# Performance work log

Hardware: AMD Instinct MI355X
Metric: run time of the kernel (lower is better)

The kernel has to match this reference:

```python
import jax, jax.numpy as jnp
import numpy as np

B, S, D, H = 1, 2048, 2048, 16
HD = D // H  # head_dim = 128
EPS = 1e-6


def setup_inputs() -> dict:
    key = jax.random.key(0)
    ks = jax.random.split(key, 12)
    sc = 0.02
    x = jax.random.normal(ks[0], (B, S, D), jnp.float32)
    wq = jax.random.normal(ks[1], (D, D), jnp.float32) * sc
    bq = jnp.zeros((D,), jnp.float32)
    wk = jax.random.normal(ks[2], (D, D), jnp.float32) * sc
    bk = jnp.zeros((D,), jnp.float32)
    wv = jax.random.normal(ks[3], (D, D), jnp.float32) * sc
    bv = jnp.zeros((D,), jnp.float32)
    wo = jax.random.normal(ks[4], (D, D), jnp.float32) * sc
    bo = jnp.zeros((D,), jnp.float32)
    gq = jnp.ones((D,), jnp.float32)  # RMSNorm weight for q
    gk = jnp.ones((D,), jnp.float32)  # RMSNorm weight for k
    # Rotary frequency table: complex freqs = cos + i*sin, shape [S, 1, HD//2]
    pos = jnp.arange(S, dtype=jnp.float32)
    inv = 1.0 / (10000.0 ** (jnp.arange(0, HD, 2, dtype=jnp.float32) / HD))  # [HD//2]
    theta = pos[:, None] * inv[None, :]  # [S, HD//2]
    freqs_cos = jnp.cos(theta)[:, None, :]  # [S, 1, HD//2]
    freqs_sin = jnp.sin(theta)[:, None, :]
    return {"x": x, "wq": wq, "bq": bq, "wk": wk, "bk": bk, "wv": wv, "bv": bv,
            "wo": wo, "bo": bo, "gq": gq, "gk": gk,
            "freqs_cos": freqs_cos, "freqs_sin": freqs_sin}


def _rmsnorm(x, g):
    # RMSNorm over full model dim (applied BEFORE head split, as in source)
    return x * jax.lax.rsqrt(jnp.mean(x * x, axis=-1, keepdims=True) + EPS) * g


def _rope(x, cos, sin):
    # x: [B,S,D] -> (B,S,H,HD//2,2) complex pairs; complex mult by (cos + i sin)
    b, s, d = x.shape
    xr = x.reshape(b, s, H, HD // 2, 2)
    a, bb = xr[..., 0], xr[..., 1]
    # cos/sin [S,1,HD//2] broadcast against [B,S,H,HD//2]
    ra = a * cos - bb * sin
    rb = a * sin + bb * cos
    return jnp.stack([ra, rb], axis=-1).reshape(b, s, d)


def reference(x, wq, bq, wk, bk, wv, bv, wo, bo, gq, gk, freqs_cos, freqs_sin):
    b, s, d = x.shape
    q = _rope(_rmsnorm(x @ wq.T + bq, gq), freqs_cos, freqs_sin)
    k = _rope(_rmsnorm(x @ wk.T + bk, gk), freqs_cos, freqs_sin)
    v = x @ wv.T + bv
    qh = q.reshape(b, s, H, HD).transpose(0, 2, 1, 3)  # [B,H,S,HD]
    kh = k.reshape(b, s, H, HD).transpose(0, 2, 1, 3)
    vh = v.reshape(b, s, H, HD).transpose(0, 2, 1, 3)
    scores = jnp.einsum('bhqd,bhkd->bhqk', qh, kh) / np.sqrt(HD).astype(np.float32)
    attn = jax.nn.softmax(scores, axis=-1)
    out = jnp.einsum('bhqk,bhkd->bhqd', attn, vh)
    out = out.transpose(0, 2, 1, 3).reshape(b, s, d)
    return out @ wo.T + bo
```

## Files before the change

kernel.cpp:

```cpp
#include <hip/hip_runtime.h>
#include <math.h>

typedef unsigned short u16;
typedef unsigned int u32;
typedef __bf16 bf16x8 __attribute__((ext_vector_type(8)));
typedef float f32x4 __attribute__((ext_vector_type(4)));
typedef float f32x16 __attribute__((ext_vector_type(16)));

__device__ __forceinline__ u16 f2bf(float f) {
  unsigned u = __float_as_uint(f);
  u += 0x7fff + ((u >> 16) & 1);
  return (u16)(u >> 16);
}

__device__ __forceinline__ u32 cvtpk(float lo, float hi) {
  u32 r;
  asm("v_cvt_pk_bf16_f32 %0, %1, %2" : "=v"(r) : "v"(lo), "v"(hi));
  return r;
}

__device__ __forceinline__ void pswap(u32& x, u32& y) {
  asm volatile("v_permlane32_swap_b32 %0, %1" : "+v"(x), "+v"(y));
}

__device__ __forceinline__ void gload_lds16(const void* g, void* l) {
  __builtin_amdgcn_global_load_lds(
      (const __attribute__((address_space(1))) unsigned int*)g,
      (__attribute__((address_space(3))) unsigned int*)l, 16, 0, 0);
}

__global__ __launch_bounds__(256) void k_cvt5(const float* __restrict__ s0,
                                              const float* __restrict__ s1,
                                              const float* __restrict__ s2,
                                              const float* __restrict__ s3,
                                              const float* __restrict__ s4,
                                              u16* __restrict__ dx,
                                              u16* __restrict__ dqkv,
                                              u16* __restrict__ dwo) {
  const int y = blockIdx.y;
  const float* s = (y == 0) ? s0 : (y == 1) ? s1 : (y == 2) ? s2
                   : (y == 3) ? s3 : s4;
  u16* d = (y == 0) ? dx : (y == 4) ? dwo : dqkv + (size_t)(y - 1) * 4194304;
  int i = (blockIdx.x * 256 + threadIdx.x) * 4;
  float4 v = *(const float4*)(s + i);
  ushort4 o;
  o.x = f2bf(v.x); o.y = f2bf(v.y); o.z = f2bf(v.z); o.w = f2bf(v.w);
  *(ushort4*)(d + i) = o;
}

__global__ __launch_bounds__(512, 4) void k_gemm_big(const u16* __restrict__ A,
                                                     const u16* __restrict__ B,
                                                     float* __restrict__ C,
                                                     int M, int N, int K) {
  __shared__ __align__(16) char lds[2][40960];
  const int tid = threadIdx.x;
  const int wid = tid >> 6, lane = tid & 63;
  const int lr = lane & 15, lg = lane >> 4;
  const int wm = (wid >> 2) * 64, wn = (wid & 3) * 48;
  const int nbx = N / 192, nby = M >> 7;
  const int colsPerXcd = nbx >> 3;
  const int xcd = blockIdx.x & 7, idx = blockIdx.x >> 3;
  const int bx = xcd * colsPerXcd + idx / nby;
  const int by = idx % nby;
  const int bm = by * 128, bn = bx * 192;
  const int srow = tid >> 3;
  const int schunk = (tid & 7) ^ (srow & 7);
  const size_t rsK = (size_t)K * 2;
  const char* gA = (const char*)A + (size_t)(bm + srow) * rsK + schunk * 16;
  const char* gB = (const char*)B + (size_t)(bn + srow) * rsK + schunk * 16;
  char* dA = (char*)lds + wid * 1024;
  char* dB = (char*)lds + 16384 + wid * 1024;

#define STAGE(cur, k0)                                                         \
  {                                                                            \
    _Pragma("unroll") for (int i = 0; i < 2; ++i)                              \
        gload_lds16(gA + (size_t)(i * 64) * rsK + (size_t)(k0) * 2,            \
                    dA + (cur) * 40960 + i * 8192);                            \
    _Pragma("unroll") for (int i = 0; i < 3; ++i)                              \
        gload_lds16(gB + (size_t)(i * 64) * rsK + (size_t)(k0) * 2,            \
                    dB + (cur) * 40960 + i * 8192);                            \
  }

  f32x4 acc[4][3] = {};
  STAGE(0, 0);
  STAGE(1, 64);
  asm volatile("s_waitcnt vmcnt(5)" ::: "memory");
  __builtin_amdgcn_s_barrier();
  const int NT = K >> 6;
  int cur = 0;
  const int rsw = (lr & 7);
  for (int t = 0; t < NT; ++t) {
    const char* La = (const char*)lds + cur * 40960;
    const char* Lb = La + 16384;
    bf16x8 af[4][2], bfr[3][2];
#pragma unroll
    for (int mi = 0; mi < 4; ++mi)
#pragma unroll
      for (int kk = 0; kk < 2; ++kk)
        af[mi][kk] = *(const bf16x8*)(La + (wm + mi * 16 + lr) * 128 +
                                      (((kk * 4 + lg) ^ rsw) * 16));
#pragma unroll
    for (int ni = 0; ni < 3; ++ni)
#pragma unroll
      for (int kk = 0; kk < 2; ++kk)
        bfr[ni][kk] = *(const bf16x8*)(Lb + (wn + ni * 16 + lr) * 128 +
                                       (((kk * 4 + lg) ^ rsw) * 16));
    asm volatile("s_waitcnt lgkmcnt(0)" ::: "memory");
    __builtin_amdgcn_s_barrier();
    if (t + 2 < NT) STAGE(cur, (t + 2) << 6);
    __builtin_amdgcn_s_setprio(1);
#pragma unroll
    for (int kk = 0; kk < 2; ++kk)
#pragma unroll
      for (int mi = 0; mi < 4; ++mi)
#pragma unroll
        for (int ni = 0; ni < 3; ++ni)
          acc[mi][ni] = __builtin_amdgcn_mfma_f32_16x16x32_bf16(
              af[mi][kk], bfr[ni][kk], acc[mi][ni], 0, 0, 0);
    __builtin_amdgcn_s_setprio(0);
    if (t + 2 < NT)
      asm volatile("s_waitcnt vmcnt(5)" ::: "memory");
    else
      asm volatile("s_waitcnt vmcnt(0)" ::: "memory");
    __builtin_amdgcn_s_barrier();
    cur ^= 1;
  }
#undef STAGE
#pragma unroll
  for (int mi = 0; mi < 4; ++mi)
#pragma unroll
    for (int ni = 0; ni < 3; ++ni)
#pragma unroll
      for (int j = 0; j < 4; ++j)
        C[(size_t)(bm + wm + mi * 16 + lg * 4 + j) * N + bn + wn + ni * 16 + lr] =
            acc[mi][ni][j];
}

__global__ __launch_bounds__(256, 2) void k_gemm_pipe(const u16* __restrict__ A,
                                                      const u16* __restrict__ B,
                                                      const float* __restrict__ bias,
                                                      float* __restrict__ C,
                                                      int M, int N, int K) {
  __shared__ __align__(16) char lds[2][24576];
  const int tid = threadIdx.x;
  const int wid = tid >> 6, lane = tid & 63;
  const int lr = lane & 15, lg = lane >> 4;
  const int wm = (wid >> 1) * 64, wn = (wid & 1) * 32;
  const int nbx = N >> 6, nby = M >> 7;
  const int colsPerXcd = nbx >> 3;
  const int xcd = blockIdx.x & 7, idx = blockIdx.x >> 3;
  const int bx = xcd * colsPerXcd + idx / nby;
  const int by = idx % nby;
  const int bm = by * 128, bn = bx * 64;
  const int srow = tid >> 3;
  const int schunk = (tid & 7) ^ (srow & 7);
  const size_t rsK = (size_t)K * 2;
  const char* gA = (const char*)A + (size_t)(bm + srow) * rsK + schunk * 16;
  const char* gB = (const char*)B + (size_t)(bn + srow) * rsK + schunk * 16;
  char* dA = (char*)lds + wid * 1024;
  char* dB = (char*)lds + 16384 + wid * 1024;

#define STAGE(cur, k0)                                                         \
  {                                                                            \
    _Pragma("unroll") for (int i = 0; i < 4; ++i)                              \
        gload_lds16(gA + (size_t)(i * 32) * rsK + (size_t)(k0) * 2,            \
                    dA + (cur) * 24576 + i * 4096);                            \
    _Pragma("unroll") for (int i = 0; i < 2; ++i)                              \
        gload_lds16(gB + (size_t)(i * 32) * rsK + (size_t)(k0) * 2,            \
                    dB + (cur) * 24576 + i * 4096);                            \
  }

  f32x4 acc[4][2] = {};
  STAGE(0, 0);
  STAGE(1, 64);
  asm volatile("s_waitcnt vmcnt(6)" ::: "memory");
  __builtin_amdgcn_s_barrier();
  const int NT = K >> 6;
  int cur = 0;
  const int rsw = (lr & 7);
  for (int t = 0; t < NT; ++t) {
    const char* La = (const char*)lds + cur * 24576;
    const char* Lb = La + 16384;
    bf16x8 af[4][2], bfr[2][2];
#pragma unroll
    for (int mi = 0; mi < 4; ++mi)
#pragma unroll
      for (int kk = 0; kk < 2; ++kk)
        af[mi][kk] = *(const bf16x8*)(La + (wm + mi * 16 + lr) * 128 +
                                      (((kk * 4 + lg) ^ rsw) * 16));
#pragma unroll
    for (int ni = 0; ni < 2; ++ni)
#pragma unroll
      for (int kk = 0; kk < 2; ++kk)
        bfr[ni][kk] = *(const bf16x8*)(Lb + (wn + ni * 16 + lr) * 128 +
                                       (((kk * 4 + lg) ^ rsw) * 16));
    asm volatile("s_waitcnt lgkmcnt(0)" ::: "memory");
    __builtin_amdgcn_s_barrier();
    if (t + 2 < NT) STAGE(cur, (t + 2) << 6);
    __builtin_amdgcn_s_setprio(1);
#pragma unroll
    for (int kk = 0; kk < 2; ++kk)
#pragma unroll
      for (int mi = 0; mi < 4; ++mi)
#pragma unroll
        for (int ni = 0; ni < 2; ++ni)
          acc[mi][ni] = __builtin_amdgcn_mfma_f32_16x16x32_bf16(
              af[mi][kk], bfr[ni][kk], acc[mi][ni], 0, 0, 0);
    __builtin_amdgcn_s_setprio(0);
    if (t + 2 < NT)
      asm volatile("s_waitcnt vmcnt(6)" ::: "memory");
    else
      asm volatile("s_waitcnt vmcnt(0)" ::: "memory");
    __builtin_amdgcn_s_barrier();
    cur ^= 1;
  }
#undef STAGE
#pragma unroll
  for (int mi = 0; mi < 4; ++mi)
#pragma unroll
    for (int ni = 0; ni < 2; ++ni) {
      int col = bn + wn + ni * 16 + lr;
      float bb = bias[col];
#pragma unroll
      for (int j = 0; j < 4; ++j)
        C[(size_t)(bm + wm + mi * 16 + lg * 4 + j) * N + col] =
            acc[mi][ni][j] + bb;
    }
}

__global__ __launch_bounds__(256) void k_rmsnorm_rope(
    const float* __restrict__ qkv, const float* __restrict__ bq,
    const float* __restrict__ bk, const float* __restrict__ gq,
    const float* __restrict__ gk, const float* __restrict__ fcos,
    const float* __restrict__ fsin, u16* __restrict__ qb, u16* __restrict__ kb) {
  const int s = blockIdx.x, which = blockIdx.y;
  const int t = threadIdx.x;
  const float* src = qkv + (size_t)s * 6144 + which * 2048;
  const float* bias = which ? bk : bq;
  const float* g = which ? gk : gq;
  u16* dst = (which ? kb : qb) + (size_t)s * 2048;
  const int c0 = t * 8;
  float4 a0 = *(const float4*)(src + c0);
  float4 a1 = *(const float4*)(src + c0 + 4);
  float4 b0 = *(const float4*)(bias + c0);
  float4 b1 = *(const float4*)(bias + c0 + 4);
  float v[8];
  v[0] = a0.x + b0.x; v[1] = a0.y + b0.y; v[2] = a0.z + b0.z; v[3] = a0.w + b0.w;
  v[4] = a1.x + b1.x; v[5] = a1.y + b1.y; v[6] = a1.z + b1.z; v[7] = a1.w + b1.w;
  float ss = 0.f;
#pragma unroll
  for (int j = 0; j < 8; ++j) ss += v[j] * v[j];
#pragma unroll
  for (int m = 1; m < 64; m <<= 1) ss += __shfl_xor(ss, m);
  __shared__ float red[4];
  if ((t & 63) == 0) red[t >> 6] = ss;
  __syncthreads();
  float r = rsqrtf((red[0] + red[1] + red[2] + red[3]) * (1.0f / 2048.0f) + 1e-6f);
  if (!which) r *= 0.08838834764831843f * 1.4426950408889634f;
  float4 g0 = *(const float4*)(g + c0);
  float4 g1 = *(const float4*)(g + c0 + 4);
  float gg[8] = {g0.x, g0.y, g0.z, g0.w, g1.x, g1.y, g1.z, g1.w};
  const int p0 = (c0 & 127) >> 1;
  u16 o[8];
#pragma unroll
  for (int j = 0; j < 4; ++j) {
    float a = v[2 * j] * r * gg[2 * j];
    float b = v[2 * j + 1] * r * gg[2 * j + 1];
    float co = fcos[s * 64 + p0 + j], si = fsin[s * 64 + p0 + j];
    o[2 * j]     = f2bf(a * co - b * si);
    o[2 * j + 1] = f2bf(a * si + b * co);
  }
  ushort4 q0; q0.x = o[0]; q0.y = o[1]; q0.z = o[2]; q0.w = o[3];
  ushort4 q1; q1.x = o[4]; q1.y = o[5]; q1.z = o[6]; q1.w = o[7];
  *(ushort4*)(dst + c0) = q0;
  *(ushort4*)(dst + c0 + 4) = q1;
}

__global__ __launch_bounds__(256) void k_transpose_v(const float* __restrict__ qkv,
                                                     const float* __restrict__ bv,
                                                     u16* __restrict__ vT) {
  __shared__ float tile[64][65];
  const int s0 = blockIdx.x * 64, d0 = blockIdx.y * 64;
  const int t = threadIdx.x;
  const int tc = (t & 15) * 4, tr = t >> 4;
  float4 bb = *(const float4*)(bv + d0 + tc);
#pragma unroll
  for (int i = 0; i < 4; ++i) {
    int sr = tr + i * 16;
    float4 x = *(const float4*)(qkv + (size_t)(s0 + sr) * 6144 + 4096 + d0 + tc);
    tile[sr][tc + 0] = x.x + bb.x;
    tile[sr][tc + 1] = x.y + bb.y;
    tile[sr][tc + 2] = x.z + bb.z;
    tile[sr][tc + 3] = x.w + bb.w;
  }
  __syncthreads();
#pragma unroll
  for (int i = 0; i < 4; ++i) {
    int dr = tr + i * 16;
    ushort4 o;
    o.x = f2bf(tile[tc + 0][dr]);
    o.y = f2bf(tile[tc + 1][dr]);
    o.z = f2bf(tile[tc + 2][dr]);
    o.w = f2bf(tile[tc + 3][dr]);
    *(ushort4*)(vT + (size_t)(d0 + dr) * 2048 + s0 + tc) = o;
  }
}

__global__ __launch_bounds__(256, 2) void k_attn(const u16* __restrict__ qb,
                                                 const u16* __restrict__ kb,
                                                 const u16* __restrict__ vT,
                                                 float* __restrict__ opart,
                                                 float* __restrict__ ml) {
  __shared__ __align__(16) char Ks[2][16384];
  __shared__ __align__(16) char Vs[2][16384];
  const int bid = blockIdx.x;
  const int xcd = bid & 7, j = bid >> 3;
  const int h = xcd * 2 + (j & 1);
  const int qt = (j >> 1) & 15;
  const int ks = j >> 5;
  const int tid = threadIdx.x;
  const int wid = tid >> 6, lane = tid & 63;
  const int l31 = lane & 31, hi = lane >> 5;
  const int q0w = qt * 128 + wid * 32;
  const char* kbB = (const char*)kb;
  const char* vTB = (const char*)vT;
  const int krow = tid >> 4;
  const int kc = (tid & 15) ^ krow;
  const int vrow = tid >> 3;
  const int vc = (tid & 7) ^ (vrow & 7);

#define STAGE(buf, k0)                                                         \
  {                                                                            \
    _Pragma("unroll") for (int i = 0; i < 4; ++i)                              \
        gload_lds16(kbB + (size_t)((k0) + i * 16 + krow) * 4096 + h * 256 +    \
                        kc * 16,                                               \
                    (char*)Ks + (buf) * 16384 + i * 4096 + wid * 1024);        \
    _Pragma("unroll") for (int i = 0; i < 4; ++i)                              \
        gload_lds16(vTB + (size_t)(h * 128 + i * 32 + vrow) * 4096 +           \
                        (size_t)(k0) * 2 + vc * 16,                            \
                    (char*)Vs + (buf) * 16384 + i * 4096 + wid * 1024);        \
  }

  bf16x8 qf[8];
#pragma unroll
  for (int ds = 0; ds < 8; ++ds)
    qf[ds] = *(const bf16x8*)(qb + (size_t)(q0w + l31) * 2048 + h * 128 +
                              ds * 16 + hi * 8);
  f32x16 o[4] = {};
  float mrun = -3.0e38f, lsum = 0.f;
  const int kbeg = ks * 1024;
  const int ksw = l31 & 15, vsw = l31 & 7;
  STAGE(0, kbeg);
  __syncthreads();
  int cur = 0;
  for (int t = 0; t < 16; ++t) {
    if (t + 1 < 16) STAGE(cur ^ 1, kbeg + (t + 1) * 64);
    const char* Kc = Ks[cur];
    const char* Vc = Vs[cur];
    f32x16 p0 = {}, p1 = {};
    __builtin_amdgcn_s_setprio(1);
#pragma unroll
    for (int ds = 0; ds < 8; ++ds) {
      bf16x8 kf0 = *(const bf16x8*)(Kc + l31 * 256 + (((ds * 2 + hi) ^ ksw) * 16));
      p0 = __builtin_amdgcn_mfma_f32_32x32x16_bf16(kf0, qf[ds], p0, 0, 0, 0);
      bf16x8 kf1 = *(const bf16x8*)(Kc + (32 + l31) * 256 +
                                    (((ds * 2 + hi) ^ ksw) * 16));
      p1 = __builtin_amdgcn_mfma_f32_32x32x16_bf16(kf1, qf[ds], p1, 0, 0, 0);
    }
    __builtin_amdgcn_s_setprio(0);
    {
      float tm[8];
#pragma unroll
      for (int r = 0; r < 8; ++r)
        tm[r] = fmaxf(fmaxf(p0[2 * r], p0[2 * r + 1]),
                      fmaxf(p1[2 * r], p1[2 * r + 1]));
#pragma unroll
      for (int s = 4; s > 0; s >>= 1)
#pragma unroll
        for (int r = 0; r < s; ++r) tm[r] = fmaxf(tm[r], tm[r + s]);
      float pm = fmaxf(tm[0], __shfl_xor(tm[0], 32));
      if (!__all(pm <= mrun + 8.0f)) {
        float nm = fmaxf(mrun, pm);
        float fv = __builtin_amdgcn_exp2f(mrun - nm);
#pragma unroll
        for (int dt = 0; dt < 4; ++dt) o[dt] *= fv;
        lsum *= fv;
        mrun = nm;
      }
    }
    {
#pragma unroll
      for (int r = 0; r < 16; ++r) p0[r] = __builtin_amdgcn_exp2f(p0[r] - mrun);
#pragma unroll
      for (int r = 0; r < 16; ++r) p1[r] = __builtin_amdgcn_exp2f(p1[r] - mrun);
      float ts[8];
#pragma unroll
      for (int r = 0; r < 8; ++r)
        ts[r] = (p0[2 * r] + p0[2 * r + 1]) + (p1[2 * r] + p1[2 * r + 1]);
#pragma unroll
      for (int s = 4; s > 0; s >>= 1)
#pragma unroll
        for (int r = 0; r < s; ++r) ts[r] += ts[r + s];
      lsum += ts[0] + __shfl_xor(ts[0], 32);
    }
    bf16x8 pa[4];
#pragma unroll
    for (int sl = 0; sl < 2; ++sl) {
      u32 E0 = cvtpk(p0[8 * sl + 0], p0[8 * sl + 1]);
      u32 E1 = cvtpk(p0[8 * sl + 2], p0[8 * sl + 3]);
      u32 O0 = cvtpk(p0[8 * sl + 4], p0[8 * sl + 5]);
      u32 O1 = cvtpk(p0[8 * sl + 6], p0[8 * sl + 7]);
      pswap(E0, O0); pswap(E1, O1);
      union { u32 w[4]; bf16x8 v; } uu;
      uu.w[0] = E0; uu.w[1] = E1; uu.w[2] = O0; uu.w[3] = O1;
      pa[sl] = uu.v;
    }
#pragma unroll
    for (int sl = 0; sl < 2; ++sl) {
      u32 E0 = cvtpk(p1[8 * sl + 0], p1[8 * sl + 1]);
      u32 E1 = cvtpk(p1[8 * sl + 2], p1[8 * sl + 3]);
      u32 O0 = cvtpk(p1[8 * sl + 4], p1[8 * sl + 5]);
      u32 O1 = cvtpk(p1[8 * sl + 6], p1[8 * sl + 7]);
      pswap(E0, O0); pswap(E1, O1);
      union { u32 w[4]; bf16x8 v; } uu;
      uu.w[0] = E0; uu.w[1] = E1; uu.w[2] = O0; uu.w[3] = O1;
      pa[2 + sl] = uu.v;
    }
    __builtin_amdgcn_s_setprio(1);
#pragma unroll
    for (int s = 0; s < 4; ++s)
#pragma unroll
      for (int dt = 0; dt < 4; ++dt) {
        bf16x8 vf = *(const bf16x8*)(Vc + (dt * 32 + l31) * 128 +
                                     (((s * 2 + hi) ^ vsw) * 16));
        o[dt] = __builtin_amdgcn_mfma_f32_32x32x16_bf16(pa[s], vf, o[dt], 0, 0, 0);
      }
    __builtin_amdgcn_s_setprio(0);
    __syncthreads();
    cur ^= 1;
  }
#undef STAGE
  float* opb = opart + ((size_t)ks * 32768 + (size_t)h * 2048 + q0w) * 128 + l31;
#pragma unroll
  for (int dt = 0; dt < 4; ++dt)
#pragma unroll
    for (int r = 0; r < 16; ++r)
      opb[(size_t)((r & 3) + 8 * (r >> 2) + 4 * hi) * 128 + dt * 32] = o[dt][r];
  if (lane < 32) {
    float2 v2; v2.x = mrun; v2.y = lsum;
    *(float2*)(ml + ((size_t)ks * 32768 + (size_t)h * 2048 + q0w + l31) * 2) = v2;
  }
}

__global__ __launch_bounds__(256) void k_attn_merge(const float* __restrict__ opart,
                                                    const float* __restrict__ ml,
                                                    u16* __restrict__ ob) {
  const int r = blockIdx.x * 8 + (threadIdx.x >> 5);
  const int d0 = (threadIdx.x & 31) * 4;
  float2 ml0 = *(const float2*)(ml + (size_t)r * 2);
  float2 ml1 = *(const float2*)(ml + (size_t)(32768 + r) * 2);
  float M = fmaxf(ml0.x, ml1.x);
  float f0 = __builtin_amdgcn_exp2f(ml0.x - M);
  float f1 = __builtin_amdgcn_exp2f(ml1.x - M);
  float inv = 1.0f / (ml0.y * f0 + ml1.y * f1);
  float4 a = *(const float4*)(opart + (size_t)r * 128 + d0);
  float4 b = *(const float4*)(opart + (size_t)(32768 + r) * 128 + d0);
  int h = r >> 11, q = r & 2047;
  ushort4 o;
  o.x = f2bf((a.x * f0 + b.x * f1) * inv);
  o.y = f2bf((a.y * f0 + b.y * f1) * inv);
  o.z = f2bf((a.z * f0 + b.z * f1) * inv);
  o.w = f2bf((a.w * f0 + b.w * f1) * inv);
  *(ushort4*)(ob + (size_t)q * 2048 + h * 128 + d0) = o;
}

extern "C" void kernel_launch(void* const* d_in, const int* in_sizes, int n_in,
                              void* d_out, int out_size, void* d_ws, size_t ws_size,
                              hipStream_t stream) {
  const float* x    = (const float*)d_in[0];
  const float* wq   = (const float*)d_in[1];
  const float* bq   = (const float*)d_in[2];
  const float* wk   = (const float*)d_in[3];
  const float* bk   = (const float*)d_in[4];
  const float* wv   = (const float*)d_in[5];
  const float* bv   = (const float*)d_in[6];
  const float* wo   = (const float*)d_in[7];
  const float* bo   = (const float*)d_in[8];
  const float* gq   = (const float*)d_in[9];
  const float* gk   = (const float*)d_in[10];
  const float* fcos = (const float*)d_in[11];
  const float* fsin = (const float*)d_in[12];

  char* ws = (char*)d_ws;
  float* qkv_pre = (float*)ws;
  float* opart = (float*)ws;
  float* ml    = (float*)(ws + 33554432);
  u16* xb   = (u16*)(ws + 50331648);
  u16* wqkv = (u16*)(ws + 58720256);
  u16* qb   = (u16*)(ws + 50331648);
  u16* kb   = (u16*)(ws + 58720256);
  u16* vT   = (u16*)(ws + 67108864);
  u16* ao   = (u16*)(ws + 75497472);
  u16* wob  = (u16*)(ws + 83886080);

  k_cvt5<<<dim3(4096, 5), 256, 0, stream>>>(x, wq, wk, wv, wo, xb, wqkv, wob);

  k_gemm_big<<<512, 512, 0, stream>>>(xb, wqkv, qkv_pre, 2048, 6144, 2048);
  k_rmsnorm_rope<<<dim3(2048, 2), 256, 0, stream>>>(qkv_pre, bq, bk, gq, gk,
                                                    fcos, fsin, qb, kb);
  k_transpose_v<<<dim3(32, 32), 256, 0, stream>>>(qkv_pre, bv, vT);
  k_attn<<<512, 256, 0, stream>>>(qb, kb, vT, opart, ml);
  k_attn_merge<<<4096, 256, 0, stream>>>(opart, ml, ao);
  k_gemm_pipe<<<dim3(512), 256, 0, stream>>>(ao, wob, bo, (float*)d_out,
                                             2048, 2048, 2048);
}
```

Measured before the change: 159.1 us.

## Store QKV projection in bf16 and compute softmax row sums via MFMA

The QKV GEMM now writes its output as bf16 instead of fp32, and the RMSNorm/RoPE and V-transpose kernels read bf16. This halves the intermediate traffic for the 2048x6144 buffer. In attention, the per-row exp-sum reduction (VALU adds plus a cross-lane shuffle) is replaced by an extra MFMA against a vector of ones, accumulated in a fifth f32x16 that is extracted at the end. The bf16 intermediate adds rounding before the RMSNorm, and the ones-MFMA sums bf16-rounded probabilities while using more registers.

```diff
diff --git a/kernel.cpp b/kernel.cpp
--- a/kernel.cpp
+++ b/kernel.cpp
@@ -11,6 +11,10 @@
   unsigned u = __float_as_uint(f);
   u += 0x7fff + ((u >> 16) & 1);
   return (u16)(u >> 16);
+}
+
+__device__ __forceinline__ float b2f(u16 x) {
+  return __uint_as_float((u32)x << 16);
 }
 
 __device__ __forceinline__ u32 cvtpk(float lo, float hi) {
@@ -50,7 +54,7 @@
 
 __global__ __launch_bounds__(512, 4) void k_gemm_big(const u16* __restrict__ A,
                                                      const u16* __restrict__ B,
-                                                     float* __restrict__ C,
+                                                     u16* __restrict__ C,
                                                      int M, int N, int K) {
   __shared__ __align__(16) char lds[2][40960];
   const int tid = threadIdx.x;
@@ -133,7 +137,7 @@
 #pragma unroll
       for (int j = 0; j < 4; ++j)
         C[(size_t)(bm + wm + mi * 16 + lg * 4 + j) * N + bn + wn + ni * 16 + lr] =
-            acc[mi][ni][j];
+            f2bf(acc[mi][ni][j]);
 }
 
 __global__ __launch_bounds__(256, 2) void k_gemm_pipe(const u16* __restrict__ A,
@@ -229,24 +233,26 @@
 }
 
 __global__ __launch_bounds__(256) void k_rmsnorm_rope(
-    const float* __restrict__ qkv, const float* __restrict__ bq,
+    const u16* __restrict__ qkv, const float* __restrict__ bq,
     const float* __restrict__ bk, const float* __restrict__ gq,
     const float* __restrict__ gk, const float* __restrict__ fcos,
     const float* __restrict__ fsin, u16* __restrict__ qb, u16* __restrict__ kb) {
   const int s = blockIdx.x, which = blockIdx.y;
   const int t = threadIdx.x;
-  const float* src = qkv + (size_t)s * 6144 + which * 2048;
+  const u16* src = qkv + (size_t)s * 6144 + which * 2048;
   const float* bias = which ? bk : bq;
   const float* g = which ? gk : gq;
   u16* dst = (which ? kb : qb) + (size_t)s * 2048;
   const int c0 = t * 8;
-  float4 a0 = *(const float4*)(src + c0);
-  float4 a1 = *(const float4*)(src + c0 + 4);
+  uint4 raw = *(const uint4*)(src + c0);
+  const u16* rp = (const u16*)&raw;
   float4 b0 = *(const float4*)(bias + c0);
   float4 b1 = *(const float4*)(bias + c0 + 4);
   float v[8];
-  v[0] = a0.x + b0.x; v[1] = a0.y + b0.y; v[2] = a0.z + b0.z; v[3] = a0.w + b0.w;
-  v[4] = a1.x + b1.x; v[5] = a1.y + b1.y; v[6] = a1.z + b1.z; v[7] = a1.w + b1.w;
+  v[0] = b2f(rp[0]) + b0.x; v[1] = b2f(rp[1]) + b0.y;
+  v[2] = b2f(rp[2]) + b0.z; v[3] = b2f(rp[3]) + b0.w;
+  v[4] = b2f(rp[4]) + b1.x; v[5] = b2f(rp[5]) + b1.y;
+  v[6] = b2f(rp[6]) + b1.z; v[7] = b2f(rp[7]) + b1.w;
   float ss = 0.f;
 #pragma unroll
   for (int j = 0; j < 8; ++j) ss += v[j] * v[j];
@@ -276,7 +282,7 @@
   *(ushort4*)(dst + c0 + 4) = q1;
 }
 
-__global__ __launch_bounds__(256) void k_transpose_v(const float* __restrict__ qkv,
+__global__ __launch_bounds__(256) void k_transpose_v(const u16* __restrict__ qkv,
                                                      const float* __restrict__ bv,
                                                      u16* __restrict__ vT) {
   __shared__ float tile[64][65];
@@ -287,11 +293,11 @@
 #pragma unroll
   for (int i = 0; i < 4; ++i) {
     int sr = tr + i * 16;
-    float4 x = *(const float4*)(qkv + (size_t)(s0 + sr) * 6144 + 4096 + d0 + tc);
-    tile[sr][tc + 0] = x.x + bb.x;
-    tile[sr][tc + 1] = x.y + bb.y;
-    tile[sr][tc + 2] = x.z + bb.z;
-    tile[sr][tc + 3] = x.w + bb.w;
+    ushort4 x = *(const ushort4*)(qkv + (size_t)(s0 + sr) * 6144 + 4096 + d0 + tc);
+    tile[sr][tc + 0] = b2f(x.x) + bb.x;
+    tile[sr][tc + 1] = b2f(x.y) + bb.y;
+    tile[sr][tc + 2] = b2f(x.z) + bb.z;
+    tile[sr][tc + 3] = b2f(x.w) + bb.w;
   }
   __syncthreads();
 #pragma unroll
@@ -347,9 +353,14 @@
     qf[ds] = *(const bf16x8*)(qb + (size_t)(q0w + l31) * 2048 + h * 128 +
                               ds * 16 + hi * 8);
   f32x16 o[4] = {};
-  float mrun = -3.0e38f, lsum = 0.f;
+  f32x16 o4 = {};
+  float mrun = -3.0e38f;
   const int kbeg = ks * 1024;
   const int ksw = l31 & 15, vsw = l31 & 7;
+  union { u32 w[4]; bf16x8 v; } onesu;
+  onesu.w[0] = 0x3F803F80u; onesu.w[1] = 0x3F803F80u;
+  onesu.w[2] = 0x3F803F80u; onesu.w[3] = 0x3F803F80u;
+  const bf16x8 vones = onesu.v;
   STAGE(0, kbeg);
   __syncthreads();
   int cur = 0;
@@ -384,25 +395,14 @@
         float fv = __builtin_amdgcn_exp2f(mrun - nm);
 #pragma unroll
         for (int dt = 0; dt < 4; ++dt) o[dt] *= fv;
-        lsum *= fv;
+        o4 *= fv;
         mrun = nm;
       }
     }
-    {
-#pragma unroll
-      for (int r = 0; r < 16; ++r) p0[r] = __builtin_amdgcn_exp2f(p0[r] - mrun);
-#pragma unroll
-      for (int r = 0; r < 16; ++r) p1[r] = __builtin_amdgcn_exp2f(p1[r] - mrun);
-      float ts[8];
-#pragma unroll
-      for (int r = 0; r < 8; ++r)
-        ts[r] = (p0[2 * r] + p0[2 * r + 1]) + (p1[2 * r] + p1[2 * r + 1]);
-#pragma unroll
-      for (int s = 4; s > 0; s >>= 1)
-#pragma unroll
-        for (int r = 0; r < s; ++r) ts[r] += ts[r + s];
-      lsum += ts[0] + __shfl_xor(ts[0], 32);
-    }
+#pragma unroll
+    for (int r = 0; r < 16; ++r) p0[r] = __builtin_amdgcn_exp2f(p0[r] - mrun);
+#pragma unroll
+    for (int r = 0; r < 16; ++r) p1[r] = __builtin_amdgcn_exp2f(p1[r] - mrun);
     bf16x8 pa[4];
 #pragma unroll
     for (int sl = 0; sl < 2; ++sl) {
@@ -428,13 +428,15 @@
     }
     __builtin_amdgcn_s_setprio(1);
 #pragma unroll
-    for (int s = 0; s < 4; ++s)
+    for (int s = 0; s < 4; ++s) {
 #pragma unroll
       for (int dt = 0; dt < 4; ++dt) {
         bf16x8 vf = *(const bf16x8*)(Vc + (dt * 32 + l31) * 128 +
                                      (((s * 2 + hi) ^ vsw) * 16));
         o[dt] = __builtin_amdgcn_mfma_f32_32x32x16_bf16(pa[s], vf, o[dt], 0, 0, 0);
       }
+      o4 = __builtin_amdgcn_mfma_f32_32x32x16_bf16(pa[s], vones, o4, 0, 0, 0);
+    }
     __builtin_amdgcn_s_setprio(0);
     __syncthreads();
     cur ^= 1;
@@ -446,9 +448,17 @@
 #pragma unroll
     for (int r = 0; r < 16; ++r)
       opb[(size_t)((r & 3) + 8 * (r >> 2) + 4 * hi) * 128 + dt * 32] = o[dt][r];
-  if (lane < 32) {
-    float2 v2; v2.x = mrun; v2.y = lsum;
-    *(float2*)(ml + ((size_t)ks * 32768 + (size_t)h * 2048 + q0w + l31) * 2) = v2;
+  {
+    const int rsel = (l31 & 3) | (((l31 >> 3) & 3) << 2);
+    float cand = o4[0];
+#pragma unroll
+    for (int r = 1; r < 16; ++r) cand = (rsel == r) ? o4[r] : cand;
+    float other = __shfl_xor(cand, 32);
+    float lsum_q = (hi == ((l31 >> 2) & 1)) ? cand : other;
+    if (lane < 32) {
+      float2 v2; v2.x = mrun; v2.y = lsum_q;
+      *(float2*)(ml + ((size_t)ks * 32768 + (size_t)h * 2048 + q0w + l31) * 2) = v2;
+    }
   }
 }
 
@@ -492,7 +502,7 @@
   const float* fsin = (const float*)d_in[12];
 
   char* ws = (char*)d_ws;
-  float* qkv_pre = (float*)ws;
+  u16* qkv_pre = (u16*)ws;
   float* opart = (float*)ws;
   float* ml    = (float*)(ws + 33554432);
   u16* xb   = (u16*)(ws + 50331648);
```

Result: no change. 156.5 us (median of 2 runs) (-1.6%).
